# Kernel tuning notes

Hardware: AMD Instinct MI355X
Metric: run time of the kernel (lower is better)

The kernel has to match this reference:

```python
import jax, jax.numpy as jnp
import numpy as np

N_NODES = 50000
N_EDGES = 1000000


def _edge_conv(x, src, dst, W, b, n_nodes):
    """PyG EdgeConv: msg = nn(cat([x_i, x_j - x_i])), aggr=max over incoming edges."""
    xi = x[dst]                      # [E, C] target features
    xj = x[src]                      # [E, C] source features
    m = jnp.concatenate([xi, xj - xi], axis=-1)          # [E, 2C]
    m = jax.nn.relu(m @ W + b)                           # [E, C_out]
    out = jax.ops.segment_max(m, dst, num_segments=n_nodes)  # [N, C_out]
    # empty segments produce -inf; PyG fills with 0
    return jnp.where(jnp.isfinite(out), out, 0.0)


def setup_inputs() -> dict:
    key = jax.random.key(0)
    ks = jax.random.split(key, 12)
    x = jax.random.normal(ks[0], (N_NODES, 3), dtype=jnp.float32)
    edge_index = jax.random.randint(ks[1], (2, N_EDGES), 0, N_NODES, dtype=jnp.int64)

    def lin(k, fan_in, fan_out):
        s = 1.0 / np.sqrt(fan_in)
        kw, kb = jax.random.split(k)
        W = jax.random.uniform(kw, (fan_in, fan_out), jnp.float32, -s, s)
        b = jax.random.uniform(kb, (fan_out,), jnp.float32, -s, s)
        return W, b

    W1, b1 = lin(ks[2], 6, 64)       # conv1 MLP([3*2, 64])
    W2, b2 = lin(ks[3], 128, 128)    # conv2 MLP([64*2, 128])
    W3, b3 = lin(ks[4], 256, 512)    # conv3 MLP([128*2, 512])
    W4, b4 = lin(ks[5], 512, 256)    # lin1 MLP([512, 256])
    W5, b5 = lin(ks[6], 256, 3)      # lin1 final Linear(256, 3)
    return {"x": x, "edge_index": edge_index,
            "W1": W1, "b1": b1, "W2": W2, "b2": b2, "W3": W3, "b3": b3,
            "W4": W4, "b4": b4, "W5": W5, "b5": b5}


def reference(x, edge_index, W1, b1, W2, b2, W3, b3, W4, b4, W5, b5):
    src = edge_index[0]  # x_j
    dst = edge_index[1]  # x_i (aggregation target)
    n = x.shape[0]
    x1 = _edge_conv(x, src, dst, W1, b1, n)    # [N, 64]
    x2 = _edge_conv(x1, src, dst, W2, b2, n)   # [N, 128]
    x3 = _edge_conv(x2, src, dst, W3, b3, n)   # [N, 512]
    x4 = jax.nn.relu(x3 @ W4 + b4) @ W5 + b5   # [N, 3]
    return x + x4
```

## Files before the change

### kernel.cpp

```cpp
#include <hip/hip_runtime.h>

static constexpr int NN = 50000;
static constexpr int NE = 1000000;

typedef short bf16x8 __attribute__((ext_vector_type(8)));
typedef float f32x4 __attribute__((ext_vector_type(4)));

__device__ inline float bf2f_raw(unsigned short u) {
    return __uint_as_float(((unsigned int)u) << 16);
}
__device__ inline unsigned short f2bf(float f) {
    unsigned int u = __float_as_uint(f);
    u += 0x7fffu + ((u >> 16) & 1u);
    return (unsigned short)(u >> 16);
}
__device__ inline void fmax2(float& a0, float& a1, unsigned int v) {
    a0 = fmaxf(a0, bf2f_raw((unsigned short)(v & 0xffffu)));
    a1 = fmaxf(a1, bf2f_raw((unsigned short)(v >> 16)));
}
__device__ inline unsigned int pack2(float f0, float f1) {
    return (unsigned int)f2bf(f0) | ((unsigned int)f2bf(f1) << 16);
}
__device__ inline unsigned int addrelu2(unsigned int a, float t0, float t1) {
    float f0 = fmaxf(bf2f_raw((unsigned short)(a & 0xffffu)) + t0, 0.f);
    float f1 = fmaxf(bf2f_raw((unsigned short)(a >> 16)) + t1, 0.f);
    return pack2(f0, f1);
}


__global__ void init_out_kernel(const float* __restrict__ x, const float* __restrict__ b5,
                                float* __restrict__ out) {
    int t = blockIdx.x * blockDim.x + threadIdx.x;
    if (t < NN * 3) out[t] = x[t] + b5[t % 3];
}


__global__ void hist_kernel(const int* __restrict__ dst, int* __restrict__ deg) {
    int e = blockIdx.x * blockDim.x + threadIdx.x;
    if (e < NE) atomicAdd(&deg[dst[e]], 1);
}

__global__ __launch_bounds__(1024) void scan_kernel(const int* __restrict__ deg,
                                                    int* __restrict__ rowstart,
                                                    int* __restrict__ cursor) {
    __shared__ int wave_sums[16];
    __shared__ int carry_s;
    int tid = threadIdx.x;
    int lane = tid & 63;
    int wave = tid >> 6;
    for (int i = tid; i < NN; i += 1024) cursor[i] = 0;
    if (tid == 0) carry_s = 0;
    __syncthreads();
    for (int base = 0; base < NN; base += 1024) {
        int idx = base + tid;
        int v = (idx < NN) ? deg[idx] : 0;
        int x = v;
        #pragma unroll
        for (int off = 1; off < 64; off <<= 1) {
            int y = __shfl_up(x, off);
            if (lane >= off) x += y;
        }
        if (lane == 63) wave_sums[wave] = x;
        __syncthreads();
        if (wave == 0 && lane < 16) {
            int s = wave_sums[lane];
            #pragma unroll
            for (int off = 1; off < 16; off <<= 1) {
                int y = __shfl_up(s, off);
                if (lane >= off) s += y;
            }
            wave_sums[lane] = s;
        }
        __syncthreads();
        int wave_off = wave ? wave_sums[wave - 1] : 0;
        int chunk_total = wave_sums[15];
        int carry = carry_s;
        if (idx < NN) rowstart[idx] = carry + wave_off + x - v;
        __syncthreads();
        if (tid == 0) carry_s = carry + chunk_total;
        __syncthreads();
    }
    if (tid == 0) rowstart[NN] = carry_s;
}

__global__ void scatter_kernel(const int* __restrict__ src, const int* __restrict__ dst,
                               const int* __restrict__ rowstart, int* __restrict__ cursor,
                               int* __restrict__ csr) {
    int e = blockIdx.x * blockDim.x + threadIdx.x;
    if (e < NE) {
        int d = dst[e];
        int pos = atomicAdd(&cursor[d], 1);
        csr[rowstart[d] + pos] = src[e];
    }
}


__global__ void prep_all_kernel(const float* __restrict__ W2, const float* __restrict__ W3,
                                const float* __restrict__ W4,
                                unsigned short* __restrict__ Bt2,
                                unsigned short* __restrict__ Bt3,
                                unsigned short* __restrict__ W4t) {
    int t = blockIdx.x * blockDim.x + threadIdx.x;
    if (t < 8192) {
        int k = t / 128, c = t % 128;
        float wt = W2[k * 128 + c];
        float wb = W2[(64 + k) * 128 + c];
        Bt2[c * 64 + k] = f2bf(wt - wb);
        Bt2[(128 + c) * 64 + k] = f2bf(wb);
    } else if (t < 8192 + 65536) {
        int u = t - 8192;
        int k = u / 512, c = u % 512;
        float wt = W3[k * 512 + c];
        float wb = W3[(128 + k) * 512 + c];
        Bt3[c * 128 + k] = f2bf(wt - wb);
        Bt3[(512 + c) * 128 + k] = f2bf(wb);
    } else if (t < 8192 + 65536 + 131072) {
        int u = t - 8192 - 65536;
        int k = u / 256, n = u % 256;
        W4t[n * 512 + k] = f2bf(W4[k * 256 + n]);
    }
}


__global__ void conv1_s_kernel(const float* __restrict__ x, const float* __restrict__ W1,
                               unsigned short* __restrict__ s) {
    int t = blockIdx.x * blockDim.x + threadIdx.x;
    int i = t >> 6, c = t & 63;
    if (i >= NN) return;
    float v = x[i * 3 + 0] * W1[3 * 64 + c] + x[i * 3 + 1] * W1[4 * 64 + c] +
              x[i * 3 + 2] * W1[5 * 64 + c];
    s[t] = f2bf(v);
}


__global__ __launch_bounds__(256) void edge_fused_conv1_kernel(
    const unsigned short* __restrict__ s1, const int* __restrict__ rowstart,
    const int* __restrict__ csr, const float* __restrict__ x,
    const float* __restrict__ W1, const float* __restrict__ b1,
    unsigned short* __restrict__ x1) {
    int wid = (blockIdx.x * 256 + threadIdx.x) >> 6;
    int lane = threadIdx.x & 63;
    if (wid >= NN) return;
    int e0 = __builtin_amdgcn_readfirstlane(rowstart[wid]);
    int e1 = __builtin_amdgcn_readfirstlane(rowstart[wid + 1]);
    int h = lane >> 5, c0 = (lane & 31) * 2;
    float t0 = -INFINITY, t1 = -INFINITY;
    const unsigned short* sb = s1 + c0;
    int nedge = e1 - e0;
    for (int base = 0; base < nedge; base += 64) {
        int rem = nedge - base;
        int myj = csr[(lane < rem) ? (e0 + base + lane) : e0];
        int cnt = rem < 64 ? rem : 64;
        int cp = (cnt + 7) & ~7;
        for (int q = 0; q < cp; q += 8) {
            int j0 = __shfl(myj, q + 0 + h);
            int j1 = __shfl(myj, q + 2 + h);
            int j2 = __shfl(myj, q + 4 + h);
            int j3 = __shfl(myj, q + 6 + h);
            unsigned int v0 = *(const unsigned int*)(sb + (size_t)j0 * 64);
            unsigned int v1 = *(const unsigned int*)(sb + (size_t)j1 * 64);
            unsigned int v2 = *(const unsigned int*)(sb + (size_t)j2 * 64);
            unsigned int v3 = *(const unsigned int*)(sb + (size_t)j3 * 64);
            fmax2(t0, t1, v0);
            fmax2(t0, t1, v1);
            fmax2(t0, t1, v2);
            fmax2(t0, t1, v3);
        }
    }
    t0 = fmaxf(t0, __shfl_xor(t0, 32));
    t1 = fmaxf(t1, __shfl_xor(t1, 32));
    if (h == 0) {
        float x0 = x[wid * 3 + 0], xv1 = x[wid * 3 + 1], xv2 = x[wid * 3 + 2];
        int c1 = c0 + 1;
        float a0 = x0 * (W1[c0] - W1[192 + c0]) + xv1 * (W1[64 + c0] - W1[256 + c0]) +
                   xv2 * (W1[128 + c0] - W1[320 + c0]) + b1[c0];
        float a1 = x0 * (W1[c1] - W1[192 + c1]) + xv1 * (W1[64 + c1] - W1[256 + c1]) +
                   xv2 * (W1[128 + c1] - W1[320 + c1]) + b1[c1];
        *(unsigned int*)(x1 + (size_t)wid * 64 + c0) =
            pack2(fmaxf(a0 + t0, 0.f), fmaxf(a1 + t1, 0.f));
    }
}


__global__ __launch_bounds__(256) void edge_fused128_kernel(
    const unsigned short* __restrict__ as, const int* __restrict__ rowstart,
    const int* __restrict__ csr, unsigned short* __restrict__ xout) {
    int wid = (blockIdx.x * 256 + threadIdx.x) >> 6;
    int lane = threadIdx.x & 63;
    if (wid >= NN) return;
    int e0 = __builtin_amdgcn_readfirstlane(rowstart[wid]);
    int e1 = __builtin_amdgcn_readfirstlane(rowstart[wid + 1]);
    float t0 = -INFINITY, t1 = -INFINITY;
    const unsigned short* sb = as + 128 + (size_t)lane * 2;
    int nedge = e1 - e0;
    for (int base = 0; base < nedge; base += 64) {
        int rem = nedge - base;
        int myj = csr[(lane < rem) ? (e0 + base + lane) : e0];
        int cnt = rem < 64 ? rem : 64;
        int cp = (cnt + 7) & ~7;
        for (int q = 0; q < cp; q += 8) {
            int j0 = __shfl(myj, q + 0), j1 = __shfl(myj, q + 1);
            int j2 = __shfl(myj, q + 2), j3 = __shfl(myj, q + 3);
            int j4 = __shfl(myj, q + 4), j5 = __shfl(myj, q + 5);
            int j6 = __shfl(myj, q + 6), j7 = __shfl(myj, q + 7);
            unsigned int v0 = *(const unsigned int*)(sb + (size_t)j0 * 256);
            unsigned int v1 = *(const unsigned int*)(sb + (size_t)j1 * 256);
            unsigned int v2 = *(const unsigned int*)(sb + (size_t)j2 * 256);
            unsigned int v3 = *(const unsigned int*)(sb + (size_t)j3 * 256);
            unsigned int v4 = *(const unsigned int*)(sb + (size_t)j4 * 256);
            unsigned int v5 = *(const unsigned int*)(sb + (size_t)j5 * 256);
            unsigned int v6 = *(const unsigned int*)(sb + (size_t)j6 * 256);
            unsigned int v7 = *(const unsigned int*)(sb + (size_t)j7 * 256);
            fmax2(t0, t1, v0); fmax2(t0, t1, v1);
            fmax2(t0, t1, v2); fmax2(t0, t1, v3);
            fmax2(t0, t1, v4); fmax2(t0, t1, v5);
            fmax2(t0, t1, v6); fmax2(t0, t1, v7);
        }
    }
    unsigned int av = *(const unsigned int*)(as + (size_t)wid * 256 + lane * 2);
    *(unsigned int*)(xout + (size_t)wid * 128 + lane * 2) = addrelu2(av, t0, t1);
}


__global__ __launch_bounds__(256) void edge_fused512_kernel(
    const unsigned short* __restrict__ as, const int* __restrict__ rowstart,
    const int* __restrict__ csr, unsigned short* __restrict__ xout) {
    int wid = (blockIdx.x * 256 + threadIdx.x) >> 6;
    int lane = threadIdx.x & 63;
    if (wid >= NN) return;
    int e0 = __builtin_amdgcn_readfirstlane(rowstart[wid]);
    int e1 = __builtin_amdgcn_readfirstlane(rowstart[wid + 1]);
    float acc[8];
    #pragma unroll
    for (int v = 0; v < 8; ++v) acc[v] = -INFINITY;
    const unsigned short* sb = as + 512 + (size_t)lane * 8;
    int nedge = e1 - e0;
    for (int base = 0; base < nedge; base += 64) {
        int rem = nedge - base;
        int myj = csr[(lane < rem) ? (e0 + base + lane) : e0];
        int cnt = rem < 64 ? rem : 64;
        int cp = (cnt + 3) & ~3;
        for (int q = 0; q < cp; q += 4) {
            int j0 = __shfl(myj, q + 0), j1 = __shfl(myj, q + 1);
            int j2 = __shfl(myj, q + 2), j3 = __shfl(myj, q + 3);
            uint4 v0 = *(const uint4*)(sb + (size_t)j0 * 1024);
            uint4 v1 = *(const uint4*)(sb + (size_t)j1 * 1024);
            uint4 v2 = *(const uint4*)(sb + (size_t)j2 * 1024);
            uint4 v3 = *(const uint4*)(sb + (size_t)j3 * 1024);
            fmax2(acc[0], acc[1], v0.x); fmax2(acc[2], acc[3], v0.y);
            fmax2(acc[4], acc[5], v0.z); fmax2(acc[6], acc[7], v0.w);
            fmax2(acc[0], acc[1], v1.x); fmax2(acc[2], acc[3], v1.y);
            fmax2(acc[4], acc[5], v1.z); fmax2(acc[6], acc[7], v1.w);
            fmax2(acc[0], acc[1], v2.x); fmax2(acc[2], acc[3], v2.y);
            fmax2(acc[4], acc[5], v2.z); fmax2(acc[6], acc[7], v2.w);
            fmax2(acc[0], acc[1], v3.x); fmax2(acc[2], acc[3], v3.y);
            fmax2(acc[4], acc[5], v3.z); fmax2(acc[6], acc[7], v3.w);
        }
    }
    uint4 av = *(const uint4*)(as + (size_t)wid * 1024 + lane * 8);
    uint4 o;
    o.x = addrelu2(av.x, acc[0], acc[1]);
    o.y = addrelu2(av.y, acc[2], acc[3]);
    o.z = addrelu2(av.z, acc[4], acc[5]);
    o.w = addrelu2(av.w, acc[6], acc[7]);
    *(uint4*)(xout + (size_t)wid * 512 + lane * 8) = o;
}


__global__ __launch_bounds__(256) void mfma_gemm_kernel(
    const unsigned short* __restrict__ A, const unsigned short* __restrict__ Bt,
    const float* __restrict__ bias, int bias_n,
    unsigned short* __restrict__ C, int M, int N, int K) {
    __shared__ __align__(16) unsigned short Asl[128 * 40];
    __shared__ __align__(16) unsigned short Bsl[128 * 40];
    int tid = threadIdx.x;
    int mbase = blockIdx.y * 128, nbase = blockIdx.x * 128;
    int wave = tid >> 6, lane = tid & 63;
    int wm = (wave >> 1) * 64, wn = (wave & 1) * 64;
    int quad = lane >> 4, l16 = lane & 15;
    f32x4 acc[4][4] = {};
    for (int kb = 0; kb < K; kb += 32) {
        #pragma unroll
        for (int h = 0; h < 2; ++h) {
            int c = tid + h * 256;
            int r = c >> 2, kk = (c & 3) * 8;
            uint4 va = make_uint4(0u, 0u, 0u, 0u);
            int gr = mbase + r;
            if (gr < M) va = *(const uint4*)&A[(size_t)gr * K + kb + kk];
            *(uint4*)&Asl[r * 40 + kk] = va;
            uint4 vb = *(const uint4*)&Bt[(size_t)(nbase + r) * K + kb + kk];
            *(uint4*)&Bsl[r * 40 + kk] = vb;
        }
        __syncthreads();
        bf16x8 af[4], bfr[4];
        #pragma unroll
        for (int tt = 0; tt < 4; ++tt) {
            af[tt]  = *(const bf16x8*)&Asl[(wm + tt * 16 + l16) * 40 + quad * 8];
            bfr[tt] = *(const bf16x8*)&Bsl[(wn + tt * 16 + l16) * 40 + quad * 8];
        }
        #pragma unroll
        for (int mt = 0; mt < 4; ++mt)
            #pragma unroll
            for (int nt = 0; nt < 4; ++nt)
                acc[mt][nt] = __builtin_amdgcn_mfma_f32_16x16x32_bf16(
                    af[mt], bfr[nt], acc[mt][nt], 0, 0, 0);
        __syncthreads();
    }
    #pragma unroll
    for (int mt = 0; mt < 4; ++mt) {
        #pragma unroll
        for (int r = 0; r < 4; ++r) {
            int row = mbase + wm + mt * 16 + quad * 4 + r;
            if (row >= M) continue;
            #pragma unroll
            for (int nt = 0; nt < 4; ++nt) {
                int col = nbase + wn + nt * 16 + l16;
                float v = acc[mt][nt][r];
                if (col < bias_n) v += bias[col];
                C[(size_t)row * N + col] = f2bf(v);
            }
        }
    }
}


__global__ __launch_bounds__(256) void mfma_gemm_w5_kernel(
    const unsigned short* __restrict__ A, const unsigned short* __restrict__ Bt,
    const float* __restrict__ b4, const float* __restrict__ W5,
    float* __restrict__ out, int M, int K) {
    __shared__ __align__(16) unsigned short Asl[128 * 40];
    __shared__ __align__(16) unsigned short Bsl[128 * 40];
    int tid = threadIdx.x;
    int mbase = blockIdx.y * 128, nbase = blockIdx.x * 128;
    int wave = tid >> 6, lane = tid & 63;
    int wm = (wave >> 1) * 64, wn = (wave & 1) * 64;
    int quad = lane >> 4, l16 = lane & 15;
    f32x4 acc[4][4] = {};
    for (int kb = 0; kb < K; kb += 32) {
        #pragma unroll
        for (int h = 0; h < 2; ++h) {
            int c = tid + h * 256;
            int r = c >> 2, kk = (c & 3) * 8;
            uint4 va = make_uint4(0u, 0u, 0u, 0u);
            int gr = mbase + r;
            if (gr < M) va = *(const uint4*)&A[(size_t)gr * K + kb + kk];
            *(uint4*)&Asl[r * 40 + kk] = va;
            uint4 vb = *(const uint4*)&Bt[(size_t)(nbase + r) * K + kb + kk];
            *(uint4*)&Bsl[r * 40 + kk] = vb;
        }
        __syncthreads();
        bf16x8 af[4], bfr[4];
        #pragma unroll
        for (int tt = 0; tt < 4; ++tt) {
            af[tt]  = *(const bf16x8*)&Asl[(wm + tt * 16 + l16) * 40 + quad * 8];
            bfr[tt] = *(const bf16x8*)&Bsl[(wn + tt * 16 + l16) * 40 + quad * 8];
        }
        #pragma unroll
        for (int mt = 0; mt < 4; ++mt)
            #pragma unroll
            for (int nt = 0; nt < 4; ++nt)
                acc[mt][nt] = __builtin_amdgcn_mfma_f32_16x16x32_bf16(
                    af[mt], bfr[nt], acc[mt][nt], 0, 0, 0);
        __syncthreads();
    }
    float w5r[4][3], b4v[4];
    #pragma unroll
    for (int nt = 0; nt < 4; ++nt) {
        int col = nbase + wn + nt * 16 + l16;
        b4v[nt] = b4[col];
        w5r[nt][0] = W5[col * 3 + 0];
        w5r[nt][1] = W5[col * 3 + 1];
        w5r[nt][2] = W5[col * 3 + 2];
    }
    #pragma unroll
    for (int mt = 0; mt < 4; ++mt) {
        #pragma unroll
        for (int r = 0; r < 4; ++r) {
            int row = mbase + wm + mt * 16 + quad * 4 + r;
            float p0 = 0.f, p1 = 0.f, p2 = 0.f;
            #pragma unroll
            for (int nt = 0; nt < 4; ++nt) {
                float h = fmaxf(acc[mt][nt][r] + b4v[nt], 0.f);
                p0 += h * w5r[nt][0];
                p1 += h * w5r[nt][1];
                p2 += h * w5r[nt][2];
            }
            #pragma unroll
            for (int m = 8; m; m >>= 1) {
                p0 += __shfl_xor(p0, m);
                p1 += __shfl_xor(p1, m);
                p2 += __shfl_xor(p2, m);
            }
            if (l16 == 0 && row < M) {
                atomicAdd(&out[row * 3 + 0], p0);
                atomicAdd(&out[row * 3 + 1], p1);
                atomicAdd(&out[row * 3 + 2], p2);
            }
        }
    }
}

__global__ void fallback_copy_kernel(const float* __restrict__ x, float* __restrict__ out) {
    int t = blockIdx.x * blockDim.x + threadIdx.x;
    if (t < NN * 3) out[t] = x[t];
}


extern "C" void kernel_launch(void* const* d_in, const int* in_sizes, int n_in,
                              void* d_out, int out_size, void* d_ws, size_t ws_size,
                              hipStream_t stream) {
    const float* x  = (const float*)d_in[0];
    const int*   ei = (const int*)d_in[1];
    const float* W1 = (const float*)d_in[2];
    const float* b1 = (const float*)d_in[3];
    const float* W2 = (const float*)d_in[4];
    const float* b2 = (const float*)d_in[5];
    const float* W3 = (const float*)d_in[6];
    const float* b3 = (const float*)d_in[7];
    const float* W4 = (const float*)d_in[8];
    const float* b4 = (const float*)d_in[9];
    const float* W5 = (const float*)d_in[10];
    const float* b5 = (const float*)d_in[11];
    float* out = (float*)d_out;

    char* p = (char*)d_ws;
    auto alloc = [&](size_t bytes) -> void* {
        void* r = (void*)p;
        p += (bytes + 255) & ~(size_t)255;
        return r;
    };
    int* deg      = (int*)alloc((size_t)NN * 4);
    int* rowstart = (int*)alloc((size_t)(NN + 1) * 4);
    int* cursor   = (int*)alloc((size_t)NN * 4);
    int* csr      = (int*)alloc((size_t)NE * 4);
    unsigned short* Bt2 = (unsigned short*)alloc(256 * 64 * 2);
    unsigned short* Bt3 = (unsigned short*)alloc(1024 * 128 * 2);
    unsigned short* W4t = (unsigned short*)alloc(256 * 512 * 2);
    unsigned short* x1 = (unsigned short*)alloc((size_t)NN * 64 * 2);
    unsigned short* x2 = (unsigned short*)alloc((size_t)NN * 128 * 2);
    unsigned short* x3 = (unsigned short*)alloc((size_t)NN * 512 * 2);
    unsigned short* as_slab = (unsigned short*)alloc((size_t)NN * 1024 * 2);
    size_t need = (size_t)(p - (char*)d_ws);
    if (ws_size < need) {
        fallback_copy_kernel<<<(NN * 3 + 255) / 256, 256, 0, stream>>>(x, out);
        return;
    }
    unsigned short* s1 = as_slab;

    const int* src = ei;
    const int* dst = ei + NE;

    init_out_kernel<<<(NN * 3 + 255) / 256, 256, 0, stream>>>(x, b5, out);

    hipMemsetAsync(deg, 0, (size_t)NN * 4, stream);
    hist_kernel<<<(NE + 255) / 256, 256, 0, stream>>>(dst, deg);
    scan_kernel<<<1, 1024, 0, stream>>>(deg, rowstart, cursor);
    scatter_kernel<<<(NE + 255) / 256, 256, 0, stream>>>(src, dst, rowstart, cursor, csr);

    prep_all_kernel<<<800, 256, 0, stream>>>(W2, W3, W4, Bt2, Bt3, W4t);

    conv1_s_kernel<<<NN * 64 / 256, 256, 0, stream>>>(x, W1, s1);
    edge_fused_conv1_kernel<<<12500, 256, 0, stream>>>(s1, rowstart, csr, x, W1, b1, x1);

    mfma_gemm_kernel<<<dim3(2, 391), 256, 0, stream>>>(
        x1, Bt2, b2, 128, as_slab, NN, 256, 64);
    edge_fused128_kernel<<<12500, 256, 0, stream>>>(as_slab, rowstart, csr, x2);

    mfma_gemm_kernel<<<dim3(8, 391), 256, 0, stream>>>(
        x2, Bt3, b3, 512, as_slab, NN, 1024, 128);
    edge_fused512_kernel<<<12500, 256, 0, stream>>>(as_slab, rowstart, csr, x3);

    mfma_gemm_w5_kernel<<<dim3(2, 391), 256, 0, stream>>>(
        x3, W4t, b4, W5, out, NN, 512);
}
```

Measured before the change: 631.9 us.

## Slice edge-max aggregation across channel groups and parallelize CSR scan

Replaces the three per-layer gather-max kernels with one templated kernel where each wave handles a 32-channel slice of one node, so 16 edges are gathered at once with 16-byte loads and the partial maxima are combined with lane shuffles. Grid blocks interleave slices of the same node group, aiming for L2 reuse of the neighbor rows and more parallelism per node. Conv1 now precomputes both the self term and the neighbor term into one slab so it can use the same kernel. The single-block scan now has each thread own a contiguous chunk and does one pass instead of a serialized loop with many barriers. In exchange the csr indices are reloaded by every slice wave, and the edge loop pads to multiples of 32 edges, so low-degree nodes waste more lanes.

```diff
diff --git a/kernel.cpp b/kernel.cpp
--- a/kernel.cpp
+++ b/kernel.cpp
@@ -44,43 +44,46 @@
                                                     int* __restrict__ rowstart,
                                                     int* __restrict__ cursor) {
     __shared__ int wave_sums[16];
-    __shared__ int carry_s;
+    constexpr int CH = (NN + 1023) / 1024;
     int tid = threadIdx.x;
     int lane = tid & 63;
     int wave = tid >> 6;
     for (int i = tid; i < NN; i += 1024) cursor[i] = 0;
-    if (tid == 0) carry_s = 0;
+    int base = tid * CH;
+    int vals[CH];
+    int sum = 0;
+    #pragma unroll
+    for (int i = 0; i < CH; ++i) {
+        int idx = base + i;
+        vals[i] = (idx < NN) ? deg[idx] : 0;
+        sum += vals[i];
+    }
+    int x = sum;
+    #pragma unroll
+    for (int off = 1; off < 64; off <<= 1) {
+        int y = __shfl_up(x, off);
+        if (lane >= off) x += y;
+    }
+    if (lane == 63) wave_sums[wave] = x;
     __syncthreads();
-    for (int base = 0; base < NN; base += 1024) {
-        int idx = base + tid;
-        int v = (idx < NN) ? deg[idx] : 0;
-        int x = v;
-        #pragma unroll
-        for (int off = 1; off < 64; off <<= 1) {
-            int y = __shfl_up(x, off);
-            if (lane >= off) x += y;
-        }
-        if (lane == 63) wave_sums[wave] = x;
-        __syncthreads();
-        if (wave == 0 && lane < 16) {
-            int s = wave_sums[lane];
-            #pragma unroll
-            for (int off = 1; off < 16; off <<= 1) {
-                int y = __shfl_up(s, off);
-                if (lane >= off) s += y;
-            }
-            wave_sums[lane] = s;
-        }
-        __syncthreads();
-        int wave_off = wave ? wave_sums[wave - 1] : 0;
-        int chunk_total = wave_sums[15];
-        int carry = carry_s;
-        if (idx < NN) rowstart[idx] = carry + wave_off + x - v;
-        __syncthreads();
-        if (tid == 0) carry_s = carry + chunk_total;
-        __syncthreads();
-    }
-    if (tid == 0) rowstart[NN] = carry_s;
+    if (wave == 0 && lane < 16) {
+        int s = wave_sums[lane];
+        #pragma unroll
+        for (int off = 1; off < 16; off <<= 1) {
+            int y = __shfl_up(s, off);
+            if (lane >= off) s += y;
+        }
+        wave_sums[lane] = s;
+    }
+    __syncthreads();
+    int run = (wave ? wave_sums[wave - 1] : 0) + x - sum;
+    #pragma unroll
+    for (int i = 0; i < CH; ++i) {
+        int idx = base + i;
+        if (idx < NN) rowstart[idx] = run;
+        run += vals[i];
+    }
+    if (tid == 1023) rowstart[NN] = run;
 }
 
 __global__ void scatter_kernel(const int* __restrict__ src, const int* __restrict__ dst,
@@ -122,148 +125,80 @@
 }
 
 
-__global__ void conv1_s_kernel(const float* __restrict__ x, const float* __restrict__ W1,
-                               unsigned short* __restrict__ s) {
+__global__ void conv1_as_kernel(const float* __restrict__ x, const float* __restrict__ W1,
+                                const float* __restrict__ b1,
+                                unsigned short* __restrict__ as1) {
     int t = blockIdx.x * blockDim.x + threadIdx.x;
-    int i = t >> 6, c = t & 63;
+    int i = t >> 7, c = t & 127;
     if (i >= NN) return;
-    float v = x[i * 3 + 0] * W1[3 * 64 + c] + x[i * 3 + 1] * W1[4 * 64 + c] +
-              x[i * 3 + 2] * W1[5 * 64 + c];
-    s[t] = f2bf(v);
-}
-
-
-__global__ __launch_bounds__(256) void edge_fused_conv1_kernel(
-    const unsigned short* __restrict__ s1, const int* __restrict__ rowstart,
-    const int* __restrict__ csr, const float* __restrict__ x,
-    const float* __restrict__ W1, const float* __restrict__ b1,
-    unsigned short* __restrict__ x1) {
-    int wid = (blockIdx.x * 256 + threadIdx.x) >> 6;
+    float x0 = x[i * 3 + 0], x1 = x[i * 3 + 1], x2 = x[i * 3 + 2];
+    float v;
+    if (c < 64) {
+        v = x0 * (W1[c] - W1[192 + c]) + x1 * (W1[64 + c] - W1[256 + c]) +
+            x2 * (W1[128 + c] - W1[320 + c]) + b1[c];
+    } else {
+        int cs = c - 64;
+        v = x0 * W1[192 + cs] + x1 * W1[256 + cs] + x2 * W1[320 + cs];
+    }
+    as1[t] = f2bf(v);
+}
+
+
+template<int C, int NS>
+__global__ __launch_bounds__(256) void edge_sliced_kernel(
+    const unsigned short* __restrict__ as, const int* __restrict__ rowstart,
+    const int* __restrict__ csr, unsigned short* __restrict__ xout) {
+    constexpr int R = 2 * C;
+    int bx = blockIdx.x;
+    int slice, ng;
+    if constexpr (NS == 16) {
+        slice = ((bx & 7) << 1) + blockIdx.y;
+        ng = bx >> 3;
+    } else {
+        slice = bx % NS;
+        ng = bx / NS;
+    }
+    int node = ng * 4 + (threadIdx.x >> 6);
     int lane = threadIdx.x & 63;
-    if (wid >= NN) return;
-    int e0 = __builtin_amdgcn_readfirstlane(rowstart[wid]);
-    int e1 = __builtin_amdgcn_readfirstlane(rowstart[wid + 1]);
-    int h = lane >> 5, c0 = (lane & 31) * 2;
-    float t0 = -INFINITY, t1 = -INFINITY;
-    const unsigned short* sb = s1 + c0;
+    int g = lane >> 2, sub = lane & 3;
+    if (node >= NN) return;
+    int e0 = __builtin_amdgcn_readfirstlane(rowstart[node]);
+    int e1 = __builtin_amdgcn_readfirstlane(rowstart[node + 1]);
+    float acc[8];
+    #pragma unroll
+    for (int v = 0; v < 8; ++v) acc[v] = -INFINITY;
+    const unsigned short* sb = as + C + slice * 32 + sub * 8;
     int nedge = e1 - e0;
     for (int base = 0; base < nedge; base += 64) {
         int rem = nedge - base;
         int myj = csr[(lane < rem) ? (e0 + base + lane) : e0];
         int cnt = rem < 64 ? rem : 64;
-        int cp = (cnt + 7) & ~7;
-        for (int q = 0; q < cp; q += 8) {
-            int j0 = __shfl(myj, q + 0 + h);
-            int j1 = __shfl(myj, q + 2 + h);
-            int j2 = __shfl(myj, q + 4 + h);
-            int j3 = __shfl(myj, q + 6 + h);
-            unsigned int v0 = *(const unsigned int*)(sb + (size_t)j0 * 64);
-            unsigned int v1 = *(const unsigned int*)(sb + (size_t)j1 * 64);
-            unsigned int v2 = *(const unsigned int*)(sb + (size_t)j2 * 64);
-            unsigned int v3 = *(const unsigned int*)(sb + (size_t)j3 * 64);
-            fmax2(t0, t1, v0);
-            fmax2(t0, t1, v1);
-            fmax2(t0, t1, v2);
-            fmax2(t0, t1, v3);
-        }
-    }
-    t0 = fmaxf(t0, __shfl_xor(t0, 32));
-    t1 = fmaxf(t1, __shfl_xor(t1, 32));
-    if (h == 0) {
-        float x0 = x[wid * 3 + 0], xv1 = x[wid * 3 + 1], xv2 = x[wid * 3 + 2];
-        int c1 = c0 + 1;
-        float a0 = x0 * (W1[c0] - W1[192 + c0]) + xv1 * (W1[64 + c0] - W1[256 + c0]) +
-                   xv2 * (W1[128 + c0] - W1[320 + c0]) + b1[c0];
-        float a1 = x0 * (W1[c1] - W1[192 + c1]) + xv1 * (W1[64 + c1] - W1[256 + c1]) +
-                   xv2 * (W1[128 + c1] - W1[320 + c1]) + b1[c1];
-        *(unsigned int*)(x1 + (size_t)wid * 64 + c0) =
-            pack2(fmaxf(a0 + t0, 0.f), fmaxf(a1 + t1, 0.f));
-    }
-}
-
-
-__global__ __launch_bounds__(256) void edge_fused128_kernel(
-    const unsigned short* __restrict__ as, const int* __restrict__ rowstart,
-    const int* __restrict__ csr, unsigned short* __restrict__ xout) {
-    int wid = (blockIdx.x * 256 + threadIdx.x) >> 6;
-    int lane = threadIdx.x & 63;
-    if (wid >= NN) return;
-    int e0 = __builtin_amdgcn_readfirstlane(rowstart[wid]);
-    int e1 = __builtin_amdgcn_readfirstlane(rowstart[wid + 1]);
-    float t0 = -INFINITY, t1 = -INFINITY;
-    const unsigned short* sb = as + 128 + (size_t)lane * 2;
-    int nedge = e1 - e0;
-    for (int base = 0; base < nedge; base += 64) {
-        int rem = nedge - base;
-        int myj = csr[(lane < rem) ? (e0 + base + lane) : e0];
-        int cnt = rem < 64 ? rem : 64;
-        int cp = (cnt + 7) & ~7;
-        for (int q = 0; q < cp; q += 8) {
-            int j0 = __shfl(myj, q + 0), j1 = __shfl(myj, q + 1);
-            int j2 = __shfl(myj, q + 2), j3 = __shfl(myj, q + 3);
-            int j4 = __shfl(myj, q + 4), j5 = __shfl(myj, q + 5);
-            int j6 = __shfl(myj, q + 6), j7 = __shfl(myj, q + 7);
-            unsigned int v0 = *(const unsigned int*)(sb + (size_t)j0 * 256);
-            unsigned int v1 = *(const unsigned int*)(sb + (size_t)j1 * 256);
-            unsigned int v2 = *(const unsigned int*)(sb + (size_t)j2 * 256);
-            unsigned int v3 = *(const unsigned int*)(sb + (size_t)j3 * 256);
-            unsigned int v4 = *(const unsigned int*)(sb + (size_t)j4 * 256);
-            unsigned int v5 = *(const unsigned int*)(sb + (size_t)j5 * 256);
-            unsigned int v6 = *(const unsigned int*)(sb + (size_t)j6 * 256);
-            unsigned int v7 = *(const unsigned int*)(sb + (size_t)j7 * 256);
-            fmax2(t0, t1, v0); fmax2(t0, t1, v1);
-            fmax2(t0, t1, v2); fmax2(t0, t1, v3);
-            fmax2(t0, t1, v4); fmax2(t0, t1, v5);
-            fmax2(t0, t1, v6); fmax2(t0, t1, v7);
-        }
-    }
-    unsigned int av = *(const unsigned int*)(as + (size_t)wid * 256 + lane * 2);
-    *(unsigned int*)(xout + (size_t)wid * 128 + lane * 2) = addrelu2(av, t0, t1);
-}
-
-
-__global__ __launch_bounds__(256) void edge_fused512_kernel(
-    const unsigned short* __restrict__ as, const int* __restrict__ rowstart,
-    const int* __restrict__ csr, unsigned short* __restrict__ xout) {
-    int wid = (blockIdx.x * 256 + threadIdx.x) >> 6;
-    int lane = threadIdx.x & 63;
-    if (wid >= NN) return;
-    int e0 = __builtin_amdgcn_readfirstlane(rowstart[wid]);
-    int e1 = __builtin_amdgcn_readfirstlane(rowstart[wid + 1]);
-    float acc[8];
-    #pragma unroll
-    for (int v = 0; v < 8; ++v) acc[v] = -INFINITY;
-    const unsigned short* sb = as + 512 + (size_t)lane * 8;
-    int nedge = e1 - e0;
-    for (int base = 0; base < nedge; base += 64) {
-        int rem = nedge - base;
-        int myj = csr[(lane < rem) ? (e0 + base + lane) : e0];
-        int cnt = rem < 64 ? rem : 64;
-        int cp = (cnt + 3) & ~3;
-        for (int q = 0; q < cp; q += 4) {
-            int j0 = __shfl(myj, q + 0), j1 = __shfl(myj, q + 1);
-            int j2 = __shfl(myj, q + 2), j3 = __shfl(myj, q + 3);
-            uint4 v0 = *(const uint4*)(sb + (size_t)j0 * 1024);
-            uint4 v1 = *(const uint4*)(sb + (size_t)j1 * 1024);
-            uint4 v2 = *(const uint4*)(sb + (size_t)j2 * 1024);
-            uint4 v3 = *(const uint4*)(sb + (size_t)j3 * 1024);
+        int cp = (cnt + 31) & ~31;
+        for (int q = 0; q < cp; q += 32) {
+            int j0 = __shfl(myj, q + g);
+            int j1 = __shfl(myj, q + 16 + g);
+            uint4 v0 = *(const uint4*)(sb + (size_t)j0 * R);
+            uint4 v1 = *(const uint4*)(sb + (size_t)j1 * R);
             fmax2(acc[0], acc[1], v0.x); fmax2(acc[2], acc[3], v0.y);
             fmax2(acc[4], acc[5], v0.z); fmax2(acc[6], acc[7], v0.w);
             fmax2(acc[0], acc[1], v1.x); fmax2(acc[2], acc[3], v1.y);
             fmax2(acc[4], acc[5], v1.z); fmax2(acc[6], acc[7], v1.w);
-            fmax2(acc[0], acc[1], v2.x); fmax2(acc[2], acc[3], v2.y);
-            fmax2(acc[4], acc[5], v2.z); fmax2(acc[6], acc[7], v2.w);
-            fmax2(acc[0], acc[1], v3.x); fmax2(acc[2], acc[3], v3.y);
-            fmax2(acc[4], acc[5], v3.z); fmax2(acc[6], acc[7], v3.w);
-        }
-    }
-    uint4 av = *(const uint4*)(as + (size_t)wid * 1024 + lane * 8);
-    uint4 o;
-    o.x = addrelu2(av.x, acc[0], acc[1]);
-    o.y = addrelu2(av.y, acc[2], acc[3]);
-    o.z = addrelu2(av.z, acc[4], acc[5]);
-    o.w = addrelu2(av.w, acc[6], acc[7]);
-    *(uint4*)(xout + (size_t)wid * 512 + lane * 8) = o;
+        }
+    }
+    #pragma unroll
+    for (int m = 4; m <= 32; m <<= 1) {
+        #pragma unroll
+        for (int v = 0; v < 8; ++v) acc[v] = fmaxf(acc[v], __shfl_xor(acc[v], m));
+    }
+    if (g == 0) {
+        uint4 av = *(const uint4*)(as + (size_t)node * R + slice * 32 + sub * 8);
+        uint4 o;
+        o.x = addrelu2(av.x, acc[0], acc[1]);
+        o.y = addrelu2(av.y, acc[2], acc[3]);
+        o.z = addrelu2(av.z, acc[4], acc[5]);
+        o.w = addrelu2(av.w, acc[6], acc[7]);
+        *(uint4*)(xout + (size_t)node * C + slice * 32 + sub * 8) = o;
+    }
 }
 
 
@@ -445,7 +380,6 @@
         fallback_copy_kernel<<<(NN * 3 + 255) / 256, 256, 0, stream>>>(x, out);
         return;
     }
-    unsigned short* s1 = as_slab;
 
     const int* src = ei;
     const int* dst = ei + NE;
@@ -459,16 +393,19 @@
 
     prep_all_kernel<<<800, 256, 0, stream>>>(W2, W3, W4, Bt2, Bt3, W4t);
 
-    conv1_s_kernel<<<NN * 64 / 256, 256, 0, stream>>>(x, W1, s1);
-    edge_fused_conv1_kernel<<<12500, 256, 0, stream>>>(s1, rowstart, csr, x, W1, b1, x1);
+    conv1_as_kernel<<<NN * 128 / 256, 256, 0, stream>>>(x, W1, b1, as_slab);
+    edge_sliced_kernel<64, 2><<<dim3(2 * 12500, 1), 256, 0, stream>>>(
+        as_slab, rowstart, csr, x1);
 
     mfma_gemm_kernel<<<dim3(2, 391), 256, 0, stream>>>(
         x1, Bt2, b2, 128, as_slab, NN, 256, 64);
-    edge_fused128_kernel<<<12500, 256, 0, stream>>>(as_slab, rowstart, csr, x2);
+    edge_sliced_kernel<128, 4><<<dim3(4 * 12500, 1), 256, 0, stream>>>(
+        as_slab, rowstart, csr, x2);
 
     mfma_gemm_kernel<<<dim3(8, 391), 256, 0, stream>>>(
         x2, Bt3, b3, 512, as_slab, NN, 1024, 128);
-    edge_fused512_kernel<<<12500, 256, 0, stream>>>(as_slab, rowstart, csr, x3);
+    edge_sliced_kernel<512, 16><<<dim3(8 * 12500, 2), 256, 0, stream>>>(
+        as_slab, rowstart, csr, x3);
 
     mfma_gemm_w5_kernel<<<dim3(2, 391), 256, 0, stream>>>(
         x3, W4t, b4, W5, out, NN, 512);
```

After: 866.2 us. 37.1% more time.
